# Kernel tuning notes

Hardware: AMD Instinct MI355X
Metric: run time of the kernel (lower is better)

The kernel has to match this reference:

```python
import jax, jax.numpy as jnp
from jax import lax
import numpy as np

B, L, H, P, M = 8, 4096, 256, 512, 1024  # batch, seq_len, h_dim, ssm state dim (2*h), mlp hidden (4*h)

def _ln(x):
    m = jnp.mean(x, -1, keepdims=True)
    v = jnp.mean((x - m) ** 2, -1, keepdims=True)
    return (x - m) * lax.rsqrt(v + 1e-6)

def _mod(x, shift, scale):
    return x * (1.0 + scale[:, None, :]) + shift[:, None, :]

def _mlp(x, w1, b1, w2, b2):
    h = jax.nn.gelu(x @ w1.T + b1, approximate=False)
    return h @ w2.T + b2

def _s5(u, Lre, Lim, Bre, Bim, Cre, Cim, D, log_step):
    # Diagonal S5 with ZOH discretization and bidirectional parallel associative scan.
    Lam = Lre + 1j * Lim                                     # [P] complex diagonal A
    dt = jnp.exp(log_step)                                   # [P]
    Lbar = jnp.exp(Lam * dt)                                 # [P]
    Bbar = ((Lbar - 1.0) / Lam)[:, None] * (Bre + 1j * Bim)  # [P,H]
    Bu = jnp.einsum('blh,ph->blp', u + 0j, Bbar)             # [B,L,P] complex
    a = jnp.broadcast_to(Lbar, Bu.shape)
    def comb(e1, e2):
        a1, b1 = e1
        a2, b2 = e2
        return a2 * a1, a2 * b1 + b2
    xs_f = lax.associative_scan(comb, (a, Bu), axis=1)[1]
    xs_b = lax.associative_scan(comb, (a, Bu[:, ::-1]), axis=1)[1][:, ::-1]
    xs = jnp.concatenate([xs_f, xs_b], axis=-1)              # [B,L,2P]
    y = 2.0 * jnp.real(jnp.einsum('blp,hp->blh', xs, Cre + 1j * Cim))
    return y + D * u

def setup_inputs() -> dict:
    key = jax.random.key(0)
    kit = iter(jax.random.split(key, 80))
    def nrm(shape, s=1.0):
        return jax.random.normal(next(kit), shape, dtype=jnp.float32) * s
    d = {}
    d['ppg_signal'] = nrm((B, H, L))
    d['x_t'] = nrm((B, H, L))
    d['cond'] = nrm((B, H))
    d['w_ada'] = nrm((12 * H, H), 0.02)
    d['b_ada'] = jnp.zeros((12 * H,), jnp.float32)
    for pfx in ('ppg', 'tgt'):
        d[pfx + '_Lre'] = -0.5 - jax.random.uniform(next(kit), (P,), dtype=jnp.float32)
        d[pfx + '_Lim'] = jnp.pi * jnp.arange(P, dtype=jnp.float32)
        d[pfx + '_Bre'] = nrm((P, H), 1.0 / np.sqrt(H))
        d[pfx + '_Bim'] = nrm((P, H), 1.0 / np.sqrt(H))
        d[pfx + '_Cre'] = nrm((H, 2 * P), 1.0 / np.sqrt(2 * P))
        d[pfx + '_Cim'] = nrm((H, 2 * P), 1.0 / np.sqrt(2 * P))
        d[pfx + '_D'] = nrm((H,))
        d[pfx + '_log_step'] = jnp.log(0.001) + (jnp.log(0.1) - jnp.log(0.001)) * jax.random.uniform(next(kit), (P,), dtype=jnp.float32)
    for pfx in ('pre_ppg', 'mlp_ppg', 'pre_tgt', 'post_tgt', 'mlp_tgt'):
        d[pfx + '_w1'] = nrm((M, H), 0.02)
        d[pfx + '_b1'] = jnp.zeros((M,), jnp.float32)
        d[pfx + '_w2'] = nrm((H, M), 0.02)
        d[pfx + '_b2'] = jnp.zeros((H,), jnp.float32)
    return d

def reference(ppg_signal, x_t, cond, w_ada, b_ada, ppg_Lre, ppg_Lim, ppg_Bre, ppg_Bim, ppg_Cre, ppg_Cim, ppg_D, ppg_log_step, tgt_Lre, tgt_Lim, tgt_Bre, tgt_Bim, tgt_Cre, tgt_Cim, tgt_D, tgt_log_step, pre_ppg_w1, pre_ppg_b1, pre_ppg_w2, pre_ppg_b2, mlp_ppg_w1, mlp_ppg_b1, mlp_ppg_w2, mlp_ppg_b2, pre_tgt_w1, pre_tgt_b1, pre_tgt_w2, pre_tgt_b2, post_tgt_w1, post_tgt_b1, post_tgt_w2, post_tgt_b2, mlp_tgt_w1, mlp_tgt_b1, mlp_tgt_w2, mlp_tgt_b2):
    p = jnp.swapaxes(ppg_signal, 1, 2)  # [B,L,H]
    t = jnp.swapaxes(x_t, 1, 2)         # [B,L,H]
    mods = jnp.split(jax.nn.silu(cond) @ w_ada.T + b_ada, 12, axis=1)
    (sh_sp, sc_sp, g_sp, sh_mp, sc_mp, g_mp, sh_st, sc_st, g_st, sh_mt, sc_mt, g_mt) = mods
    res_p = p
    ppg_cond = g_sp[:, None, :] * _s5(_mod(_ln(p), sh_sp, sc_sp), ppg_Lre, ppg_Lim, ppg_Bre, ppg_Bim, ppg_Cre, ppg_Cim, ppg_D, ppg_log_step)
    p = res_p + ppg_cond
    p = res_p + g_mp[:, None, :] * _mlp(_mod(_ln(p), sh_mp, sc_mp), mlp_ppg_w1, mlp_ppg_b1, mlp_ppg_w2, mlp_ppg_b2)
    res_t = t
    tc = g_st[:, None, :] * _s5(_mod(_ln(t), sh_st, sc_st), tgt_Lre, tgt_Lim, tgt_Bre, tgt_Bim, tgt_Cre, tgt_Cim, tgt_D, tgt_log_step)
    pc = _mlp(ppg_cond, pre_ppg_w1, pre_ppg_b1, pre_ppg_w2, pre_ppg_b2)
    tc = _mlp(tc, pre_tgt_w1, pre_tgt_b1, pre_tgt_w2, pre_tgt_b2) + pc
    tc = _mlp(tc, post_tgt_w1, post_tgt_b1, post_tgt_w2, post_tgt_b2)
    t2 = res_t + tc
    dx = res_t + g_mt[:, None, :] * _mlp(_mod(_ln(t2), sh_mt, sc_mt), mlp_tgt_w1, mlp_tgt_b1, mlp_tgt_w2, mlp_tgt_b2)
    return jnp.swapaxes(p, 1, 2), jnp.swapaxes(dx, 1, 2)
```

## Files before the change

kernel.cpp:

```cpp
#include <hip/hip_runtime.h>
#include <hip/hip_bf16.h>
#include <math.h>

typedef unsigned short u16;
typedef unsigned int   u32;
typedef __bf16 bf16x8 __attribute__((ext_vector_type(8)));
typedef u16    u16x8  __attribute__((ext_vector_type(8)));
typedef float  f32x4  __attribute__((ext_vector_type(4)));

#define B_  8
#define L_  4096
#define H_  256
#define P_  512
#define NC_ 32
#define CH_ 128

__device__ __forceinline__ float bf2f(u16 v) { return __uint_as_float(((u32)v) << 16); }
__device__ __forceinline__ u16 f2bf(float f) {
  u32 u = __float_as_uint(f);
  u32 r = u + 0x7FFFu + ((u >> 16) & 1u);
  return (u16)(r >> 16);
}

__device__ __forceinline__ void gload16(const u16* g, u16* l) {
  __builtin_amdgcn_global_load_lds((const __attribute__((address_space(1))) u32*)g,
                                   (__attribute__((address_space(3))) u32*)l, 16, 0, 0);
}

struct F2B10 { const float* s[10]; };
__global__ __launch_bounds__(256) void k_f2b10(F2B10 a, u16* __restrict__ dst) {
  int g = blockIdx.y;
  int i = (blockIdx.x << 8) + threadIdx.x;
  dst[(size_t)g * 262144 + i] = f2bf(a.s[g][i]);
}

__global__ __launch_bounds__(256) void k_mods(const float* __restrict__ cond,
                                              const float* __restrict__ wada,
                                              const float* __restrict__ bada,
                                              float* __restrict__ mods) {
  __shared__ float s[256];
  int b = blockIdx.y;
  int j = (blockIdx.x << 8) + threadIdx.x;
  float c = cond[b * 256 + threadIdx.x];
  s[threadIdx.x] = c / (1.0f + expf(-c));
  __syncthreads();
  float acc = bada[j];
  const float* wr = wada + (size_t)j * 256;
#pragma unroll 8
  for (int k = 0; k < 256; ++k) acc += s[k] * wr[k];
  mods[b * 3072 + j] = acc;
}

__global__ __launch_bounds__(256) void k_tin(const float* __restrict__ in, u16* __restrict__ out,
                                             int b0) {
  __shared__ u16 tile[64][65];
  int b = blockIdx.z, l0 = blockIdx.x << 6, h0 = blockIdx.y << 6;
  int tx = threadIdx.x, ty = threadIdx.y;
#pragma unroll
  for (int i = 0; i < 16; ++i) {
    int h = h0 + ty + i * 4;
    tile[ty + i * 4][tx] = f2bf(in[((size_t)(b0 + b) * 256 + h) * 4096 + l0 + tx]);
  }
  __syncthreads();
#pragma unroll
  for (int i = 0; i < 16; ++i) {
    int l = l0 + ty + i * 4;
    out[((size_t)b * 4096 + l) * 256 + h0 + tx] = tile[tx][ty + i * 4];
  }
}
__global__ __launch_bounds__(256) void k_tout(const u16* __restrict__ src, float* __restrict__ dst) {
  __shared__ u16 tile[64][65];
  int b = blockIdx.z, l0 = blockIdx.x << 6, h0 = blockIdx.y << 6;
  int tx = threadIdx.x, ty = threadIdx.y;
#pragma unroll
  for (int i = 0; i < 16; ++i) {
    int l = l0 + ty + i * 4;
    tile[ty + i * 4][tx] = src[((size_t)b * 4096 + l) * 256 + h0 + tx];
  }
  __syncthreads();
#pragma unroll
  for (int i = 0; i < 16; ++i) {
    int h = h0 + ty + i * 4;
    dst[((size_t)b * 256 + h) * 4096 + l0 + tx] = bf2f(tile[tx][ty + i * 4]);
  }
}

__global__ __launch_bounds__(256) void k_lnmod(const u16* __restrict__ X, u16* __restrict__ U,
                                               const float* __restrict__ mods,
                                               int sh_off, int sc_off, int b0) {
  int t = blockIdx.x, tid = threadIdx.x;
  int b = b0 + (t >> 12);
  float x = bf2f(X[(size_t)t * 256 + tid]);
  float s1 = x, s2 = x * x;
#pragma unroll
  for (int off = 32; off; off >>= 1) { s1 += __shfl_xor(s1, off); s2 += __shfl_xor(s2, off); }
  __shared__ float red[8];
  int w = tid >> 6;
  if ((tid & 63) == 0) { red[w * 2] = s1; red[w * 2 + 1] = s2; }
  __syncthreads();
  s1 = red[0] + red[2] + red[4] + red[6];
  s2 = red[1] + red[3] + red[5] + red[7];
  float m = s1 * (1.0f / 256.0f);
  float v = fmaxf(s2 * (1.0f / 256.0f) - m * m, 0.0f);
  float r = rsqrtf(v + 1e-6f);
  float sc = mods[b * 3072 + sc_off + tid];
  float sh = mods[b * 3072 + sh_off + tid];
  U[(size_t)t * 256 + tid] = f2bf((x - m) * r * (1.0f + sc) + sh);
}

__global__ __launch_bounds__(256) void k_wb2(const float* Lre0, const float* Lim0, const float* ls0,
                                             const float* Bre0, const float* Bim0, u16* WB0,
                                             const float* Lre1, const float* Lim1, const float* ls1,
                                             const float* Bre1, const float* Bim1, u16* WB1) {
  int s = blockIdx.y;
  const float* Lre = s ? Lre1 : Lre0;
  const float* Lim = s ? Lim1 : Lim0;
  const float* ls  = s ? ls1  : ls0;
  const float* Bre = s ? Bre1 : Bre0;
  const float* Bim = s ? Bim1 : Bim0;
  u16* WB = s ? WB1 : WB0;
  int p = blockIdx.x, h = threadIdx.x;
  float lre = Lre[p], lim = Lim[p];
  float dt = expf(ls[p]);
  float er = expf(lre * dt), sn, cs;
  sincosf(lim * dt, &sn, &cs);
  float ar = er * cs - 1.0f, ai = er * sn;
  float den = lre * lre + lim * lim;
  float cr = (ar * lre + ai * lim) / den;
  float ci = (ai * lre - ar * lim) / den;
  float br = Bre[p * 256 + h], bi = Bim[p * 256 + h];
  WB[(size_t)(2 * p) * 256 + h]     = f2bf(cr * br - ci * bi);
  WB[(size_t)(2 * p + 1) * 256 + h] = f2bf(cr * bi + ci * br);
}

__global__ __launch_bounds__(256) void k_wc2(const float* Cre0, const float* Cim0, u16* W0,
                                             const float* Cre1, const float* Cim1, u16* W1) {
  int s = blockIdx.y;
  const float* Cre = s ? Cre1 : Cre0;
  const float* Cim = s ? Cim1 : Cim0;
  u16* W = s ? W1 : W0;
  int idx = (blockIdx.x << 8) + threadIdx.x;
  int h = idx >> 11, k = idx & 2047;
  int sc = ((k >> 10) << 9) + ((k & 1023) >> 1);
  float v = (k & 1) ? -2.0f * Cim[h * 1024 + sc] : 2.0f * Cre[h * 1024 + sc];
  W[idx] = f2bf(v);
}

__device__ __forceinline__ float2 lbar_of(const float* Lre, const float* Lim, const float* lstep,
                                          int p, float mul) {
  float dt = expf(lstep[p]) * mul;
  float er = expf(Lre[p] * dt), sn, cs;
  sincosf(Lim[p] * dt, &sn, &cs);
  return make_float2(er * cs, er * sn);
}

__global__ __launch_bounds__(256) void k_scanA(const float* Lre, const float* Lim, const float* lstep,
                                               const u16* __restrict__ Bu,
                                               float2* __restrict__ carries, int dir) {
  int g = (blockIdx.x << 8) + threadIdx.x;
  int p = g & 511, chunk = (g >> 9) & 31, bl = g >> 14;
  float2 a = lbar_of(Lre, Lim, lstep, p, 1.0f);
  float xr = 0.f, xi = 0.f;
  int l = dir ? (4095 - chunk * CH_) : (chunk * CH_);
  int step = dir ? -1 : 1;
  const u32* bup = (const u32*)Bu + (((size_t)((bl << 12) + l)) << 9) + p;
  long pstep = (long)step << 9;
#pragma unroll 8
  for (int j = 0; j < CH_; ++j) {
    u32 w = *bup;
    float br = bf2f((u16)(w & 0xFFFF)), bi = bf2f((u16)(w >> 16));
    float nr = a.x * xr - a.y * xi + br;
    float ni = a.x * xi + a.y * xr + bi;
    xr = nr; xi = ni;
    bup += pstep;
  }
  carries[g] = make_float2(xr, xi);
}

__global__ __launch_bounds__(256) void k_scanB(const float* Lre, const float* Lim, const float* lstep,
                                               const float2* __restrict__ carries,
                                               float2* __restrict__ carryin) {
  int g = (blockIdx.x << 8) + threadIdx.x;
  int p = g & 511, bl = g >> 9;
  float2 an = lbar_of(Lre, Lim, lstep, p, (float)CH_);
  float xr = 0.f, xi = 0.f;
  size_t base = (size_t)bl * 16384 + p;
  for (int c = 0; c < NC_; ++c) {
    size_t idx = base + (size_t)c * 512;
    carryin[idx] = make_float2(xr, xi);
    float2 E = carries[idx];
    float nr = an.x * xr - an.y * xi + E.x;
    float ni = an.x * xi + an.y * xr + E.y;
    xr = nr; xi = ni;
  }
}

__global__ __launch_bounds__(256) void k_scanC(const float* Lre, const float* Lim, const float* lstep,
                                               const u16* __restrict__ Bu,
                                               const float2* __restrict__ carryin,
                                               u32* __restrict__ xs, int dir) {
  int g = (blockIdx.x << 8) + threadIdx.x;
  int p = g & 511, chunk = (g >> 9) & 31, bl = g >> 14;
  float2 a = lbar_of(Lre, Lim, lstep, p, 1.0f);
  float2 c0 = carryin[g];
  float xr = c0.x, xi = c0.y;
  int l = dir ? (4095 - chunk * CH_) : (chunk * CH_);
  int step = dir ? -1 : 1;
  const u32* bup = (const u32*)Bu + (((size_t)((bl << 12) + l)) << 9) + p;
  u32* op = xs + (((size_t)((bl << 12) + l)) << 9) + p;
  long pstep = (long)step << 9;
#pragma unroll 4
  for (int j = 0; j < CH_; ++j) {
    u32 w = *bup;
    float br = bf2f((u16)(w & 0xFFFF)), bi = bf2f((u16)(w >> 16));
    float nr = a.x * xr - a.y * xi + br;
    float ni = a.x * xi + a.y * xr + bi;
    xr = nr; xi = ni;
    *op = (u32)f2bf(xr) | ((u32)f2bf(xi) << 16);
    bup += pstep;
    op  += pstep;
  }
}

template <int MODE>
__global__ __launch_bounds__(256, 8) void gemm64_bt(const u16* __restrict__ A, const u16* __restrict__ W,
                                                    u16* __restrict__ out, int M, int N, int K,
                                                    const float* __restrict__ bias,
                                                    const float* __restrict__ gmods, int g_off, int b0,
                                                    const u16* __restrict__ res, const u16* __restrict__ add) {
  __shared__ __align__(16) u16 sA[64 * 64];
  __shared__ __align__(16) u16 sB[64 * 64];
  const int tid = threadIdx.x;
  const int wave = tid >> 6, lane = tid & 63;
  const int m0 = blockIdx.y << 6, n0 = blockIdx.x << 6;
  const int wm = (wave >> 1) << 5, wn = (wave & 1) << 5;
  const int lr = lane & 15;
  const int lk = (lane >> 4) << 3;
  const int swz = (lr & 7) << 3;

  f32x4 acc[2][2];
#pragma unroll
  for (int i = 0; i < 2; ++i)
#pragma unroll
    for (int j = 0; j < 2; ++j) acc[i][j] = (f32x4){0.f, 0.f, 0.f, 0.f};

  const int gr = lane >> 3;
  const int gc = ((lane & 7) ^ gr) << 3;
  const u16* Ag = A + (size_t)(m0 + wave * 16 + gr) * K + gc;
  const u16* Wg = W + (size_t)(n0 + wave * 16 + gr) * K + gc;
  u16* lA = &sA[(wave * 16) * 64];
  u16* lB = &sB[(wave * 16) * 64];

  for (int k0 = 0; k0 < K; k0 += 64) {
    __syncthreads();
    gload16(Ag + k0, lA);
    gload16(Ag + (size_t)8 * K + k0, lA + 8 * 64);
    gload16(Wg + k0, lB);
    gload16(Wg + (size_t)8 * K + k0, lB + 8 * 64);
    __syncthreads();
#pragma unroll
    for (int kk = 0; kk < 64; kk += 32) {
      bf16x8 af[2], bfr[2];
#pragma unroll
      for (int i = 0; i < 2; ++i)
        af[i] = *(const bf16x8*)&sA[(wm + i * 16 + lr) * 64 + ((kk + lk) ^ swz)];
#pragma unroll
      for (int j = 0; j < 2; ++j)
        bfr[j] = *(const bf16x8*)&sB[(wn + j * 16 + lr) * 64 + ((kk + lk) ^ swz)];
#pragma unroll
      for (int i = 0; i < 2; ++i)
#pragma unroll
        for (int j = 0; j < 2; ++j)
          acc[i][j] = __builtin_amdgcn_mfma_f32_16x16x32_bf16(af[i], bfr[j], acc[i][j], 0, 0, 0);
    }
  }

  const int lq = lane >> 4;
#pragma unroll
  for (int i = 0; i < 2; ++i)
#pragma unroll
    for (int j = 0; j < 2; ++j)
#pragma unroll
      for (int r = 0; r < 4; ++r) {
        int m = m0 + wm + i * 16 + lq * 4 + r;
        int n = n0 + wn + j * 16 + lr;
        float v = acc[i][j][r];
        size_t o = (size_t)m * N + n;
        if (MODE == 0) {
          out[o] = f2bf(v);
        } else if (MODE == 1) {
          float z = v + bias[n];
          out[o] = f2bf(0.5f * z * (1.0f + erff(z * 0.70710678118f)));
        } else if (MODE == 2) {
          out[o] = f2bf(v + bias[n]);
        } else if (MODE == 3) {
          out[o] = f2bf(v + bias[n] + bf2f(add[o]));
        } else if (MODE == 4) {
          out[o] = f2bf(v + bias[n] + bf2f(res[o]));
        } else {
          int bb = b0 + (m >> 12);
          float g = gmods[bb * 3072 + g_off + n];
          out[o] = f2bf(bf2f(res[o]) + g * (v + bias[n]));
        }
      }
}

__global__ __launch_bounds__(256, 8) void gemm64_cat(const u16* __restrict__ A1, const u16* __restrict__ A2,
                                                     const u16* __restrict__ W, u16* __restrict__ out,
                                                     int M, int N,
                                                     const float* __restrict__ gmods, int g_off, int b0,
                                                     const u16* __restrict__ res, const u16* __restrict__ uin,
                                                     const float* __restrict__ Dv, u16* __restrict__ out2) {
  __shared__ __align__(16) u16 sA[64 * 64];
  __shared__ __align__(16) u16 sB[64 * 64];
  const int tid = threadIdx.x;
  const int wave = tid >> 6, lane = tid & 63;
  const int m0 = blockIdx.y << 6, n0 = blockIdx.x << 6;
  const int wm = (wave >> 1) << 5, wn = (wave & 1) << 5;
  const int lr = lane & 15;
  const int lk = (lane >> 4) << 3;
  const int swz = (lr & 7) << 3;

  f32x4 acc[2][2];
#pragma unroll
  for (int i = 0; i < 2; ++i)
#pragma unroll
    for (int j = 0; j < 2; ++j) acc[i][j] = (f32x4){0.f, 0.f, 0.f, 0.f};

  const int gr = lane >> 3;
  const int gc = ((lane & 7) ^ gr) << 3;
  const u16* A1g = A1 + (size_t)(m0 + wave * 16 + gr) * 1024 + gc;
  const u16* A2g = A2 + (size_t)(m0 + wave * 16 + gr) * 1024 + gc;
  const u16* Wg  = W  + (size_t)(n0 + wave * 16 + gr) * 2048 + gc;
  u16* lA = &sA[(wave * 16) * 64];
  u16* lB = &sB[(wave * 16) * 64];

  for (int k0 = 0; k0 < 2048; k0 += 64) {
    const u16* Ag = (k0 < 1024) ? (A1g + k0) : (A2g + (k0 - 1024));
    __syncthreads();
    gload16(Ag, lA);
    gload16(Ag + (size_t)8 * 1024, lA + 8 * 64);
    gload16(Wg + k0, lB);
    gload16(Wg + (size_t)8 * 2048 + k0, lB + 8 * 64);
    __syncthreads();
#pragma unroll
    for (int kk = 0; kk < 64; kk += 32) {
      bf16x8 af[2], bfr[2];
#pragma unroll
      for (int i = 0; i < 2; ++i)
        af[i] = *(const bf16x8*)&sA[(wm + i * 16 + lr) * 64 + ((kk + lk) ^ swz)];
#pragma unroll
      for (int j = 0; j < 2; ++j)
        bfr[j] = *(const bf16x8*)&sB[(wn + j * 16 + lr) * 64 + ((kk + lk) ^ swz)];
#pragma unroll
      for (int i = 0; i < 2; ++i)
#pragma unroll
        for (int j = 0; j < 2; ++j)
          acc[i][j] = __builtin_amdgcn_mfma_f32_16x16x32_bf16(af[i], bfr[j], acc[i][j], 0, 0, 0);
    }
  }

  const int lq = lane >> 4;
#pragma unroll
  for (int i = 0; i < 2; ++i)
#pragma unroll
    for (int j = 0; j < 2; ++j)
#pragma unroll
      for (int r = 0; r < 4; ++r) {
        int m = m0 + wm + i * 16 + lq * 4 + r;
        int n = n0 + wn + j * 16 + lr;
        size_t o = (size_t)m * N + n;
        int bb = b0 + (m >> 12);
        float g = gmods[bb * 3072 + g_off + n];
        float c1 = g * (acc[i][j][r] + Dv[n] * bf2f(uin[o]));
        out[o] = f2bf(c1);
        if (out2) out2[o] = f2bf(bf2f(res[o]) + c1);
      }
}

extern "C" void kernel_launch(void* const* d_in, const int* in_sizes, int n_in,
                              void* d_out, int out_size, void* d_ws, size_t ws_size,
                              hipStream_t stream) {
  (void)in_sizes; (void)n_in; (void)out_size;
  float* outp = (float*)d_out;
#define F(i) ((const float*)d_in[i])

  char* ws = (char*)d_ws;
  float*  mods    = (float*)(ws + 0x000000);
  u16*    WBp     = (u16*)(ws + 0x020000);
  u16*    WBt     = (u16*)(ws + 0x0A0000);
  u16*    WCp2    = (u16*)(ws + 0x120000);
  u16*    WCt2    = (u16*)(ws + 0x220000);
  float2* carries = (float2*)(ws + 0x320000);
  float2* carryin = (float2*)(ws + 0x420000);
  u16*    wcv     = (u16*)(ws + 0x520000);

  const int widx[10] = {21, 23, 25, 27, 29, 31, 33, 35, 37, 39};
  const u16* WV[41];
  F2B10 fb;
  for (int i = 0; i < 10; ++i) {
    fb.s[i] = F(widx[i]);
    WV[widx[i]] = wcv + (size_t)i * 262144;
  }
  k_f2b10<<<dim3(1024, 10), 256, 0, stream>>>(fb, wcv);

  int nb = 1;
  for (int cand = 8; cand >= 1; cand >>= 1) {
    size_t need = (size_t)0x1000000 + (size_t)cand * 4096 * 8192;
    if (need <= ws_size) { nb = cand; break; }
  }
  const int R = nb * 4096;
  char* big = ws + 0x1000000;
  size_t sb = (size_t)R * 512;
  u16* Pt   = (u16*)(big);
  u16* Tt   = (u16*)(big + sb);
  u16* u_   = (u16*)(big + 2 * sb);
  u16* pcnd = (u16*)(big + 3 * sb);
  u16* p1   = (u16*)(big + 4 * sb);
  u16* tcb  = (u16*)(big + 5 * sb);
  u16* tmp1 = (u16*)(big + 6 * sb);
  u16* tmp2 = (u16*)(big + 7 * sb);
  u16* Bu   = (u16*)(big + 8 * sb);
  u16* xsf  = (u16*)(big + 12 * sb);

  k_mods<<<dim3(12, 8), 256, 0, stream>>>(F(2), F(3), F(4), mods);
  k_wb2<<<dim3(512, 2), 256, 0, stream>>>(F(5), F(6), F(12), F(7), F(8), WBp,
                                          F(13), F(14), F(20), F(15), F(16), WBt);
  k_wc2<<<dim3(2048, 2), 256, 0, stream>>>(F(9), F(10), WCp2, F(17), F(18), WCt2);

  for (int b0 = 0; b0 < 8; b0 += nb) {
#define GEMM(MODE, Aa, Ww, Oo, Nn, Kk, biasp, goff, resp, addp)                                    \
  gemm64_bt<MODE><<<dim3((Nn) / 64, R / 64), 256, 0, stream>>>(                                    \
      (const u16*)(Aa), (const u16*)(Ww), (u16*)(Oo), R, (Nn), (Kk), (const float*)(biasp), mods,  \
      (goff), b0, (const u16*)(resp), (const u16*)(addp))
#define SCANS(Lr, Li, Ls, dir, dst)                                                                \
  do {                                                                                             \
    k_scanA<<<nb * 64, 256, 0, stream>>>(Lr, Li, Ls, Bu, carries, dir);                            \
    k_scanB<<<nb * 2, 256, 0, stream>>>(Lr, Li, Ls, carries, carryin);                             \
    k_scanC<<<nb * 64, 256, 0, stream>>>(Lr, Li, Ls, Bu, carryin, (u32*)(dst), dir);               \
  } while (0)

    k_tin<<<dim3(64, 4, nb), dim3(64, 4), 0, stream>>>(F(0), Pt, b0);
    k_tin<<<dim3(64, 4, nb), dim3(64, 4), 0, stream>>>(F(1), Tt, b0);

    k_lnmod<<<R, 256, 0, stream>>>(Pt, u_, mods, 0 * 256, 1 * 256, b0);
    GEMM(0, u_, WBp, Bu, 1024, 256, nullptr, 0, nullptr, nullptr);
    SCANS(F(5), F(6), F(12), 0, xsf);
    SCANS(F(5), F(6), F(12), 1, Bu);
    gemm64_cat<<<dim3(4, R / 64), 256, 0, stream>>>(xsf, Bu, WCp2, pcnd, R, 256, mods, 2 * 256,
                                                    b0, Pt, u_, F(11), p1);

    k_lnmod<<<R, 256, 0, stream>>>(p1, tmp1, mods, 3 * 256, 4 * 256, b0);
    GEMM(1, tmp1, WV[25], Bu, 1024, 256, F(26), 0, nullptr, nullptr);
    GEMM(5, Bu, WV[27], tmp2, 256, 1024, F(28), 5 * 256, Pt, nullptr);
    k_tout<<<dim3(64, 4, nb), dim3(64, 4), 0, stream>>>(tmp2, outp + (size_t)b0 * 1048576);

    k_lnmod<<<R, 256, 0, stream>>>(Tt, u_, mods, 6 * 256, 7 * 256, b0);
    GEMM(0, u_, WBt, Bu, 1024, 256, nullptr, 0, nullptr, nullptr);
    SCANS(F(13), F(14), F(20), 0, xsf);
    SCANS(F(13), F(14), F(20), 1, Bu);
    gemm64_cat<<<dim3(4, R / 64), 256, 0, stream>>>(xsf, Bu, WCt2, tcb, R, 256, mods, 8 * 256,
                                                    b0, nullptr, u_, F(19), nullptr);

    GEMM(1, pcnd, WV[21], Bu, 1024, 256, F(22), 0, nullptr, nullptr);
    GEMM(2, Bu, WV[23], tmp1, 256, 1024, F(24), 0, nullptr, nullptr);
    GEMM(1, tcb, WV[29], Bu, 1024, 256, F(30), 0, nullptr, nullptr);
    GEMM(3, Bu, WV[31], tmp2, 256, 1024, F(32), 0, nullptr, tmp1);
    GEMM(1, tmp2, WV[33], Bu, 1024, 256, F(34), 0, nullptr, nullptr);
    GEMM(4, Bu, WV[35], tcb, 256, 1024, F(36), 0, Tt, nullptr);
    k_lnmod<<<R, 256, 0, stream>>>(tcb, tmp1, mods, 9 * 256, 10 * 256, b0);
    GEMM(1, tmp1, WV[37], Bu, 1024, 256, F(38), 0, nullptr, nullptr);
    GEMM(5, Bu, WV[39], tmp2, 256, 1024, F(40), 11 * 256, Tt, nullptr);
    k_tout<<<dim3(64, 4, nb), dim3(64, 4), 0, stream>>>(tmp2, outp + 8388608 + (size_t)b0 * 1048576);

#undef GEMM
#undef SCANS
  }
#undef F
}
```

Before: 1.290 ms.

## Fuse bidirectional scan passes, merge input transposes, use 128-wide GEMM for N=256

The forward and backward chunked scans are merged. One pass computes the forward carry and the backward chunk carry, the latter by accumulating powers of the decay. A second kernel runs both carry propagations, and a third runs the forward then the backward in-place chunk scan. This halves the number of scan launches and the Bu reads per phase. The two input transposes become one launch. GEMMs with N=256, including the concat output projection, switch to a 64x128 tile kernel with more accumulators per wave, which trades occupancy for reuse of the A tile.

Measured after the change: 1.173 ms. -9.1%, faster.

```diff
diff --git a/kernel.cpp b/kernel.cpp
--- a/kernel.cpp
+++ b/kernel.cpp
@@ -51,10 +51,17 @@
   mods[b * 3072 + j] = acc;
 }
 
-__global__ __launch_bounds__(256) void k_tin(const float* __restrict__ in, u16* __restrict__ out,
-                                             int b0) {
+__global__ __launch_bounds__(256) void k_tin2(const float* __restrict__ inP,
+                                              const float* __restrict__ inT,
+                                              u16* __restrict__ Pt, u16* __restrict__ Tt,
+                                              int b0, int nb) {
   __shared__ u16 tile[64][65];
-  int b = blockIdx.z, l0 = blockIdx.x << 6, h0 = blockIdx.y << 6;
+  int z = blockIdx.z;
+  int sel = (z >= nb);
+  int b = sel ? z - nb : z;
+  const float* in = sel ? inT : inP;
+  u16* out = sel ? Tt : Pt;
+  int l0 = blockIdx.x << 6, h0 = blockIdx.y << 6;
   int tx = threadIdx.x, ty = threadIdx.y;
 #pragma unroll
   for (int i = 0; i < 16; ++i) {
@@ -154,73 +161,95 @@
   return make_float2(er * cs, er * sn);
 }
 
-__global__ __launch_bounds__(256) void k_scanA(const float* Lre, const float* Lim, const float* lstep,
-                                               const u16* __restrict__ Bu,
-                                               float2* __restrict__ carries, int dir) {
+__global__ __launch_bounds__(256) void k_scanA2(const float* Lre, const float* Lim, const float* lstep,
+                                                const u16* __restrict__ Bu,
+                                                float2* __restrict__ car_f, float2* __restrict__ car_b) {
   int g = (blockIdx.x << 8) + threadIdx.x;
-  int p = g & 511, chunk = (g >> 9) & 31, bl = g >> 14;
+  int p = g & 511, rb = (g >> 9) & 31, bl = g >> 14;
   float2 a = lbar_of(Lre, Lim, lstep, p, 1.0f);
-  float xr = 0.f, xi = 0.f;
-  int l = dir ? (4095 - chunk * CH_) : (chunk * CH_);
-  int step = dir ? -1 : 1;
-  const u32* bup = (const u32*)Bu + (((size_t)((bl << 12) + l)) << 9) + p;
-  long pstep = (long)step << 9;
-#pragma unroll 8
+  float fr = 0.f, fi = 0.f;
+  float br_ = 0.f, bi_ = 0.f;
+  float pr = 1.f, pi = 0.f;
+  const u32* bup = (const u32*)Bu + (((size_t)((bl << 12) + rb * CH_)) << 9) + p;
+#pragma unroll 4
   for (int j = 0; j < CH_; ++j) {
     u32 w = *bup;
-    float br = bf2f((u16)(w & 0xFFFF)), bi = bf2f((u16)(w >> 16));
-    float nr = a.x * xr - a.y * xi + br;
-    float ni = a.x * xi + a.y * xr + bi;
-    xr = nr; xi = ni;
-    bup += pstep;
-  }
-  carries[g] = make_float2(xr, xi);
-}
-
-__global__ __launch_bounds__(256) void k_scanB(const float* Lre, const float* Lim, const float* lstep,
-                                               const float2* __restrict__ carries,
-                                               float2* __restrict__ carryin) {
+    float er = bf2f((u16)(w & 0xFFFF)), ei = bf2f((u16)(w >> 16));
+    float nr = a.x * fr - a.y * fi + er;
+    float ni = a.x * fi + a.y * fr + ei;
+    fr = nr; fi = ni;
+    br_ += pr * er - pi * ei;
+    bi_ += pr * ei + pi * er;
+    float npr = pr * a.x - pi * a.y;
+    float npi = pr * a.y + pi * a.x;
+    pr = npr; pi = npi;
+    bup += 512;
+  }
+  car_f[g] = make_float2(fr, fi);
+  car_b[((size_t)bl << 14) + ((size_t)(31 - rb) << 9) + p] = make_float2(br_, bi_);
+}
+
+__global__ __launch_bounds__(256) void k_scanB2(const float* Lre, const float* Lim, const float* lstep,
+                                                const float2* __restrict__ car_f,
+                                                const float2* __restrict__ car_b,
+                                                float2* __restrict__ cin_f, float2* __restrict__ cin_b) {
+  int dir = blockIdx.y;
   int g = (blockIdx.x << 8) + threadIdx.x;
   int p = g & 511, bl = g >> 9;
   float2 an = lbar_of(Lre, Lim, lstep, p, (float)CH_);
+  const float2* car = dir ? car_b : car_f;
+  float2* cin = dir ? cin_b : cin_f;
   float xr = 0.f, xi = 0.f;
   size_t base = (size_t)bl * 16384 + p;
   for (int c = 0; c < NC_; ++c) {
-    size_t idx = base + (size_t)c * 512;
-    carryin[idx] = make_float2(xr, xi);
-    float2 E = carries[idx];
+    size_t src = base + (size_t)c * 512;
+    size_t dst = dir ? (base + (size_t)(31 - c) * 512) : src;
+    cin[dst] = make_float2(xr, xi);
+    float2 E = car[src];
     float nr = an.x * xr - an.y * xi + E.x;
     float ni = an.x * xi + an.y * xr + E.y;
     xr = nr; xi = ni;
   }
 }
 
-__global__ __launch_bounds__(256) void k_scanC(const float* Lre, const float* Lim, const float* lstep,
-                                               const u16* __restrict__ Bu,
-                                               const float2* __restrict__ carryin,
-                                               u32* __restrict__ xs, int dir) {
+__global__ __launch_bounds__(256) void k_scanC2(const float* Lre, const float* Lim, const float* lstep,
+                                                u16* __restrict__ Bu,
+                                                const float2* __restrict__ cin_f,
+                                                const float2* __restrict__ cin_b,
+                                                u32* __restrict__ xsf) {
   int g = (blockIdx.x << 8) + threadIdx.x;
-  int p = g & 511, chunk = (g >> 9) & 31, bl = g >> 14;
+  int p = g & 511, rb = (g >> 9) & 31, bl = g >> 14;
   float2 a = lbar_of(Lre, Lim, lstep, p, 1.0f);
-  float2 c0 = carryin[g];
+  size_t rowbase = (((size_t)((bl << 12) + rb * CH_)) << 9) + p;
+  const u32* bup = (const u32*)Bu + rowbase;
+  u32* xop = xsf + rowbase;
+  float2 c0 = cin_f[g];
   float xr = c0.x, xi = c0.y;
-  int l = dir ? (4095 - chunk * CH_) : (chunk * CH_);
-  int step = dir ? -1 : 1;
-  const u32* bup = (const u32*)Bu + (((size_t)((bl << 12) + l)) << 9) + p;
-  u32* op = xs + (((size_t)((bl << 12) + l)) << 9) + p;
-  long pstep = (long)step << 9;
 #pragma unroll 4
   for (int j = 0; j < CH_; ++j) {
     u32 w = *bup;
-    float br = bf2f((u16)(w & 0xFFFF)), bi = bf2f((u16)(w >> 16));
-    float nr = a.x * xr - a.y * xi + br;
-    float ni = a.x * xi + a.y * xr + bi;
+    float er = bf2f((u16)(w & 0xFFFF)), ei = bf2f((u16)(w >> 16));
+    float nr = a.x * xr - a.y * xi + er;
+    float ni = a.x * xi + a.y * xr + ei;
     xr = nr; xi = ni;
-    *op = (u32)f2bf(xr) | ((u32)f2bf(xi) << 16);
-    bup += pstep;
-    op  += pstep;
-  }
-}
+    *xop = (u32)f2bf(xr) | ((u32)f2bf(xi) << 16);
+    bup += 512; xop += 512;
+  }
+  u32* bwp = (u32*)Bu + rowbase + ((size_t)(CH_ - 1) << 9);
+  c0 = cin_b[g];
+  xr = c0.x; xi = c0.y;
+#pragma unroll 4
+  for (int j = 0; j < CH_; ++j) {
+    u32 w = *bwp;
+    float er = bf2f((u16)(w & 0xFFFF)), ei = bf2f((u16)(w >> 16));
+    float nr = a.x * xr - a.y * xi + er;
+    float ni = a.x * xi + a.y * xr + ei;
+    xr = nr; xi = ni;
+    *bwp = (u32)f2bf(xr) | ((u32)f2bf(xi) << 16);
+    bwp -= 512;
+  }
+}
+
 
 template <int MODE>
 __global__ __launch_bounds__(256, 8) void gemm64_bt(const u16* __restrict__ A, const u16* __restrict__ W,
@@ -305,57 +334,63 @@
       }
 }
 
-__global__ __launch_bounds__(256, 8) void gemm64_cat(const u16* __restrict__ A1, const u16* __restrict__ A2,
+template <int MODE>
+__global__ __launch_bounds__(256, 4) void gemm128_bt(const u16* __restrict__ A, const u16* __restrict__ A2,
                                                      const u16* __restrict__ W, u16* __restrict__ out,
-                                                     int M, int N,
+                                                     int M, int N, int K,
+                                                     const float* __restrict__ bias,
                                                      const float* __restrict__ gmods, int g_off, int b0,
-                                                     const u16* __restrict__ res, const u16* __restrict__ uin,
-                                                     const float* __restrict__ Dv, u16* __restrict__ out2) {
+                                                     const u16* __restrict__ res, const u16* __restrict__ add,
+                                                     const u16* __restrict__ uin, const float* __restrict__ Dv,
+                                                     u16* __restrict__ out2) {
   __shared__ __align__(16) u16 sA[64 * 64];
-  __shared__ __align__(16) u16 sB[64 * 64];
+  __shared__ __align__(16) u16 sB[128 * 64];
   const int tid = threadIdx.x;
   const int wave = tid >> 6, lane = tid & 63;
-  const int m0 = blockIdx.y << 6, n0 = blockIdx.x << 6;
-  const int wm = (wave >> 1) << 5, wn = (wave & 1) << 5;
+  const int m0 = blockIdx.y << 6, n0 = blockIdx.x << 7;
+  const int wm = (wave >> 1) << 5;
+  const int wn = (wave & 1) << 6;
   const int lr = lane & 15;
   const int lk = (lane >> 4) << 3;
   const int swz = (lr & 7) << 3;
 
-  f32x4 acc[2][2];
+  f32x4 acc[2][4];
 #pragma unroll
   for (int i = 0; i < 2; ++i)
 #pragma unroll
-    for (int j = 0; j < 2; ++j) acc[i][j] = (f32x4){0.f, 0.f, 0.f, 0.f};
-
+    for (int j = 0; j < 4; ++j) acc[i][j] = (f32x4){0.f, 0.f, 0.f, 0.f};
+
+  const int As = (MODE == 6) ? 1024 : K;
   const int gr = lane >> 3;
   const int gc = ((lane & 7) ^ gr) << 3;
-  const u16* A1g = A1 + (size_t)(m0 + wave * 16 + gr) * 1024 + gc;
-  const u16* A2g = A2 + (size_t)(m0 + wave * 16 + gr) * 1024 + gc;
-  const u16* Wg  = W  + (size_t)(n0 + wave * 16 + gr) * 2048 + gc;
+  const u16* Ag  = A + (size_t)(m0 + wave * 16 + gr) * As + gc;
+  const u16* A2g = (MODE == 6) ? (A2 + (size_t)(m0 + wave * 16 + gr) * 1024 + gc) : nullptr;
+  const u16* Wg  = W + (size_t)(n0 + wave * 32 + gr) * K + gc;
   u16* lA = &sA[(wave * 16) * 64];
-  u16* lB = &sB[(wave * 16) * 64];
-
-  for (int k0 = 0; k0 < 2048; k0 += 64) {
-    const u16* Ag = (k0 < 1024) ? (A1g + k0) : (A2g + (k0 - 1024));
+  u16* lB = &sB[(wave * 32) * 64];
+
+  for (int k0 = 0; k0 < K; k0 += 64) {
+    const u16* Asrc = (MODE == 6 && k0 >= 1024) ? (A2g + (k0 - 1024)) : (Ag + k0);
     __syncthreads();
-    gload16(Ag, lA);
-    gload16(Ag + (size_t)8 * 1024, lA + 8 * 64);
-    gload16(Wg + k0, lB);
-    gload16(Wg + (size_t)8 * 2048 + k0, lB + 8 * 64);
+    gload16(Asrc, lA);
+    gload16(Asrc + (size_t)8 * As, lA + 8 * 64);
+#pragma unroll
+    for (int i = 0; i < 4; ++i)
+      gload16(Wg + (size_t)(i * 8) * K + k0, lB + i * 8 * 64);
     __syncthreads();
 #pragma unroll
     for (int kk = 0; kk < 64; kk += 32) {
-      bf16x8 af[2], bfr[2];
+      bf16x8 af[2], bfr[4];
 #pragma unroll
       for (int i = 0; i < 2; ++i)
         af[i] = *(const bf16x8*)&sA[(wm + i * 16 + lr) * 64 + ((kk + lk) ^ swz)];
 #pragma unroll
-      for (int j = 0; j < 2; ++j)
+      for (int j = 0; j < 4; ++j)
         bfr[j] = *(const bf16x8*)&sB[(wn + j * 16 + lr) * 64 + ((kk + lk) ^ swz)];
 #pragma unroll
       for (int i = 0; i < 2; ++i)
 #pragma unroll
-        for (int j = 0; j < 2; ++j)
+        for (int j = 0; j < 4; ++j)
           acc[i][j] = __builtin_amdgcn_mfma_f32_16x16x32_bf16(af[i], bfr[j], acc[i][j], 0, 0, 0);
     }
   }
@@ -364,17 +399,30 @@
 #pragma unroll
   for (int i = 0; i < 2; ++i)
 #pragma unroll
-    for (int j = 0; j < 2; ++j)
+    for (int j = 0; j < 4; ++j)
 #pragma unroll
       for (int r = 0; r < 4; ++r) {
         int m = m0 + wm + i * 16 + lq * 4 + r;
         int n = n0 + wn + j * 16 + lr;
+        float v = acc[i][j][r];
         size_t o = (size_t)m * N + n;
-        int bb = b0 + (m >> 12);
-        float g = gmods[bb * 3072 + g_off + n];
-        float c1 = g * (acc[i][j][r] + Dv[n] * bf2f(uin[o]));
-        out[o] = f2bf(c1);
-        if (out2) out2[o] = f2bf(bf2f(res[o]) + c1);
+        if (MODE == 2) {
+          out[o] = f2bf(v + bias[n]);
+        } else if (MODE == 3) {
+          out[o] = f2bf(v + bias[n] + bf2f(add[o]));
+        } else if (MODE == 4) {
+          out[o] = f2bf(v + bias[n] + bf2f(res[o]));
+        } else if (MODE == 5) {
+          int bb = b0 + (m >> 12);
+          float g = gmods[bb * 3072 + g_off + n];
+          out[o] = f2bf(bf2f(res[o]) + g * (v + bias[n]));
+        } else if (MODE == 6) {
+          int bb = b0 + (m >> 12);
+          float g = gmods[bb * 3072 + g_off + n];
+          float c1 = g * (v + Dv[n] * bf2f(uin[o]));
+          out[o] = f2bf(c1);
+          if (out2) out2[o] = f2bf(bf2f(res[o]) + c1);
+        }
       }
 }
 
@@ -386,14 +434,16 @@
 #define F(i) ((const float*)d_in[i])
 
   char* ws = (char*)d_ws;
-  float*  mods    = (float*)(ws + 0x000000);
-  u16*    WBp     = (u16*)(ws + 0x020000);
-  u16*    WBt     = (u16*)(ws + 0x0A0000);
-  u16*    WCp2    = (u16*)(ws + 0x120000);
-  u16*    WCt2    = (u16*)(ws + 0x220000);
-  float2* carries = (float2*)(ws + 0x320000);
-  float2* carryin = (float2*)(ws + 0x420000);
-  u16*    wcv     = (u16*)(ws + 0x520000);
+  float*  mods  = (float*)(ws + 0x000000);
+  u16*    WBp   = (u16*)(ws + 0x020000);
+  u16*    WBt   = (u16*)(ws + 0x0A0000);
+  u16*    WCp2  = (u16*)(ws + 0x120000);
+  u16*    WCt2  = (u16*)(ws + 0x220000);
+  float2* car_f = (float2*)(ws + 0x320000);
+  float2* car_b = (float2*)(ws + 0x420000);
+  float2* cin_f = (float2*)(ws + 0x520000);
+  float2* cin_b = (float2*)(ws + 0x620000);
+  u16*    wcv   = (u16*)(ws + 0x720000);
 
   const int widx[10] = {21, 23, 25, 27, 29, 31, 33, 35, 37, 39};
   const u16* WV[41];
@@ -430,25 +480,34 @@
 
   for (int b0 = 0; b0 < 8; b0 += nb) {
 #define GEMM(MODE, Aa, Ww, Oo, Nn, Kk, biasp, goff, resp, addp)                                    \
-  gemm64_bt<MODE><<<dim3((Nn) / 64, R / 64), 256, 0, stream>>>(                                    \
-      (const u16*)(Aa), (const u16*)(Ww), (u16*)(Oo), R, (Nn), (Kk), (const float*)(biasp), mods,  \
-      (goff), b0, (const u16*)(resp), (const u16*)(addp))
-#define SCANS(Lr, Li, Ls, dir, dst)                                                                \
   do {                                                                                             \
-    k_scanA<<<nb * 64, 256, 0, stream>>>(Lr, Li, Ls, Bu, carries, dir);                            \
-    k_scanB<<<nb * 2, 256, 0, stream>>>(Lr, Li, Ls, carries, carryin);                             \
-    k_scanC<<<nb * 64, 256, 0, stream>>>(Lr, Li, Ls, Bu, carryin, (u32*)(dst), dir);               \
+    if ((Nn) == 256)                                                                               \
+      gemm128_bt<MODE><<<dim3(2, R / 64), 256, 0, stream>>>(                                       \
+          (const u16*)(Aa), nullptr, (const u16*)(Ww), (u16*)(Oo), R, (Nn), (Kk),                  \
+          (const float*)(biasp), mods, (goff), b0, (const u16*)(resp), (const u16*)(addp),         \
+          nullptr, nullptr, nullptr);                                                              \
+    else                                                                                           \
+      gemm64_bt<MODE><<<dim3((Nn) / 64, R / 64), 256, 0, stream>>>(                                \
+          (const u16*)(Aa), (const u16*)(Ww), (u16*)(Oo), R, (Nn), (Kk), (const float*)(biasp),    \
+          mods, (goff), b0, (const u16*)(resp), (const u16*)(addp));                               \
   } while (0)
-
-    k_tin<<<dim3(64, 4, nb), dim3(64, 4), 0, stream>>>(F(0), Pt, b0);
-    k_tin<<<dim3(64, 4, nb), dim3(64, 4), 0, stream>>>(F(1), Tt, b0);
+#define SCANS2(Lr, Li, Ls)                                                                         \
+  do {                                                                                             \
+    k_scanA2<<<nb * 64, 256, 0, stream>>>(Lr, Li, Ls, Bu, car_f, car_b);                           \
+    k_scanB2<<<dim3(nb * 2, 2), 256, 0, stream>>>(Lr, Li, Ls, car_f, car_b, cin_f, cin_b);         \
+    k_scanC2<<<nb * 64, 256, 0, stream>>>(Lr, Li, Ls, Bu, cin_f, cin_b, (u32*)xsf);                \
+  } while (0)
+#define CAT(Ww, Oo, goff, resp, uinp, Dp, o2)                                                      \
+  gemm128_bt<6><<<dim3(2, R / 64), 256, 0, stream>>>(                                              \
+      (const u16*)xsf, (const u16*)Bu, (const u16*)(Ww), (u16*)(Oo), R, 256, 2048, nullptr, mods,  \
+      (goff), b0, (const u16*)(resp), nullptr, (const u16*)(uinp), (const float*)(Dp), (u16*)(o2))
+
+    k_tin2<<<dim3(64, 4, 2 * nb), dim3(64, 4), 0, stream>>>(F(0), F(1), Pt, Tt, b0, nb);
 
     k_lnmod<<<R, 256, 0, stream>>>(Pt, u_, mods, 0 * 256, 1 * 256, b0);
     GEMM(0, u_, WBp, Bu, 1024, 256, nullptr, 0, nullptr, nullptr);
-    SCANS(F(5), F(6), F(12), 0, xsf);
-    SCANS(F(5), F(6), F(12), 1, Bu);
-    gemm64_cat<<<dim3(4, R / 64), 256, 0, stream>>>(xsf, Bu, WCp2, pcnd, R, 256, mods, 2 * 256,
-                                                    b0, Pt, u_, F(11), p1);
+    SCANS2(F(5), F(6), F(12));
+    CAT(WCp2, pcnd, 2 * 256, Pt, u_, F(11), p1);
 
     k_lnmod<<<R, 256, 0, stream>>>(p1, tmp1, mods, 3 * 256, 4 * 256, b0);
     GEMM(1, tmp1, WV[25], Bu, 1024, 256, F(26), 0, nullptr, nullptr);
@@ -457,10 +516,8 @@
 
     k_lnmod<<<R, 256, 0, stream>>>(Tt, u_, mods, 6 * 256, 7 * 256, b0);
     GEMM(0, u_, WBt, Bu, 1024, 256, nullptr, 0, nullptr, nullptr);
-    SCANS(F(13), F(14), F(20), 0, xsf);
-    SCANS(F(13), F(14), F(20), 1, Bu);
-    gemm64_cat<<<dim3(4, R / 64), 256, 0, stream>>>(xsf, Bu, WCt2, tcb, R, 256, mods, 8 * 256,
-                                                    b0, nullptr, u_, F(19), nullptr);
+    SCANS2(F(13), F(14), F(20));
+    CAT(WCt2, tcb, 8 * 256, nullptr, u_, F(19), nullptr);
 
     GEMM(1, pcnd, WV[21], Bu, 1024, 256, F(22), 0, nullptr, nullptr);
     GEMM(2, Bu, WV[23], tmp1, 256, 1024, F(24), 0, nullptr, nullptr);
@@ -474,7 +531,8 @@
     k_tout<<<dim3(64, 4, nb), dim3(64, 4), 0, stream>>>(tmp2, outp + 8388608 + (size_t)b0 * 1048576);
 
 #undef GEMM
-#undef SCANS
+#undef SCANS2
+#undef CAT
   }
 #undef F
 }
```
